# Kernel tuning notes

Hardware: AMD Instinct MI355X
Metric: run time of the kernel (lower is better)

Reference implementation:

```python
import jax, jax.numpy as jnp
import numpy as np

B, S, D, V = 2, 2048, 1024, 32000
EPS_LN = 1e-5
EPS_BN = 1e-5


def setup_inputs() -> dict:
    key = jax.random.key(0)
    ks = jax.random.split(key, 8)
    s = lambda k, shape: jax.random.normal(k, shape, jnp.float32) * 0.02
    return dict(
        X=jax.random.randint(ks[0], (B, S), 0, V, dtype=jnp.int32),
        emb=s(ks[1], (V, D)),
        w_hg=s(ks[2], (D, 2 * D)),            # minGRU to_hidden_and_gate (bias-free)
        conv_w=s(ks[3], (D, D, 3)),           # Conv1d OIW
        conv_b=jnp.zeros((D,), jnp.float32),
        bn_g=jnp.ones((D,), jnp.float32), bn_b=jnp.zeros((D,), jnp.float32),
        ln_g=jnp.ones((D,), jnp.float32), ln_b=jnp.zeros((D,), jnp.float32),
        w1=s(ks[4], (D, 2 * D)), b1=jnp.zeros((2 * D,), jnp.float32),
        w2=s(ks[5], (2 * D, 2 * D)), b2=jnp.zeros((2 * D,), jnp.float32),
        w3=s(ks[6], (2 * D, V)), b3=jnp.zeros((V,), jnp.float32),
    )


def _log_g(x):
    # log of g(x) = where(x>=0, x+0.5, sigmoid(x))
    return jnp.where(x >= 0, jnp.log(jax.nn.relu(x) + 0.5), -jax.nn.softplus(-x))


def _min_gru(x, w_hg):
    # Heinsen log-space associative scan (lucidrains minGRU, expansion=1)
    hg = x @ w_hg                              # [B,S,2D]
    hidden, gate = jnp.split(hg, 2, axis=-1)
    log_coeffs = -jax.nn.softplus(gate)        # log(1 - z)
    log_values = -jax.nn.softplus(-gate) + _log_g(hidden)  # log z + log h~
    a_star = jnp.cumsum(log_coeffs, axis=1)
    log_h = a_star + jax.lax.cumlogsumexp(log_values - a_star, axis=1)
    return jnp.exp(log_h)                      # [B,S,D]


def reference(X, emb, w_hg, conv_w, conv_b, bn_g, bn_b, ln_g, ln_b,
              w1, b1, w2, b2, w3, b3):
    x = emb[X]                                 # [B,S,D]
    shortcut = x
    h = _min_gru(x, w_hg)                      # dropout rate 0 -> identity
    mu = jnp.mean(h, axis=-1, keepdims=True)
    var = jnp.mean((h - mu) ** 2, axis=-1, keepdims=True)
    h = (h - mu) / jnp.sqrt(var + EPS_LN) * ln_g + ln_b
    x = h + shortcut
    xc = jnp.transpose(x, (0, 2, 1))           # [B,D,S]
    xc = jax.lax.conv_general_dilated(
        xc, conv_w, window_strides=(1,), padding=[(1, 1)],
        dimension_numbers=('NCW', 'OIW', 'NCW')) + conv_b[None, :, None]
    m = jnp.mean(xc, axis=(0, 2), keepdims=True)       # BN training-mode stats
    v = jnp.mean((xc - m) ** 2, axis=(0, 2), keepdims=True)
    xc = (xc - m) / jnp.sqrt(v + EPS_BN) * bn_g[None, :, None] + bn_b[None, :, None]
    x = jnp.transpose(xc, (0, 2, 1))           # [B,S,D]
    x = jax.nn.relu(x @ w1 + b1)
    x = jax.nn.relu(x @ w2 + b2)
    return x @ w3 + b3                         # [B,S,V]
```

## Files before the change

### kernel.cpp

```cpp
#include <hip/hip_runtime.h>
#include <hip/hip_bf16.h>

#define B_  2
#define S_  2048
#define D_  1024
#define V_  32000
#define BS_ 4096

typedef __attribute__((ext_vector_type(4))) float f32x4;
typedef __attribute__((ext_vector_type(8))) short short8;
typedef unsigned long long u64;
typedef unsigned short u16;

__device__ __forceinline__ u16 f2bf(float x) {
  unsigned int u = __float_as_uint(x);
  u += 0x7FFFu + ((u >> 16) & 1u);
  return (u16)(u >> 16);
}
__device__ __forceinline__ u64 pack4bf(float a, float b, float c, float d) {
  return (u64)f2bf(a) | ((u64)f2bf(b) << 16) | ((u64)f2bf(c) << 32) | ((u64)f2bf(d) << 48);
}

#define GLOAD_LDS16(g, l) __builtin_amdgcn_global_load_lds( \
    (const __attribute__((address_space(1))) void*)(g),     \
    (__attribute__((address_space(3))) void*)(l), 16, 0, 0)

__device__ __forceinline__ unsigned lds_addr32(const void* p) {
  return (unsigned)(uintptr_t)(const __attribute__((address_space(3))) void*)p;
}
__device__ __forceinline__ short8 ds_read128(unsigned a) {
  short8 r;
  asm volatile("ds_read_b128 %0, %1" : "=&v"(r) : "v"(a));
  return r;
}

template<bool RELU, bool BF16OUT, bool HASBIAS>
__global__ __launch_bounds__(256) void gemm_bt(
    const u16* __restrict__ A, const u16* __restrict__ Bt,
    const float* __restrict__ bias, void* __restrict__ Cout,
    int M, int N, int K)
{
  __shared__ __attribute__((aligned(16))) u16 Alds[128 * 64];
  __shared__ __attribute__((aligned(16))) u16 Blds[128 * 64];
  const int tid = threadIdx.x;
  const int w = tid >> 6, l = tid & 63;
  const int wr = w >> 1, wc = w & 1;
  const int m0 = blockIdx.y * 128, n0 = blockIdx.x * 128;
  const int lr = l >> 3, lc = l & 7;
  const int fr = l & 15, fq = l >> 4;

  const u16* Ag = A + (size_t)(m0 + w * 8 + lr) * K + lc * 8;
  const u16* Bg = Bt + (size_t)(n0 + w * 8 + lr) * K + lc * 8;

  f32x4 acc[4][4];
#pragma unroll
  for (int i = 0; i < 4; ++i)
#pragma unroll
    for (int j = 0; j < 4; ++j) acc[i][j] = {0.f, 0.f, 0.f, 0.f};

  for (int kt = 0; kt < K; kt += 64) {
#pragma unroll
    for (int r = 0; r < 4; ++r) {
      GLOAD_LDS16(Ag + (size_t)(r * 32) * K + kt, &Alds[(r * 32 + w * 8) * 64]);
      GLOAD_LDS16(Bg + (size_t)(r * 32) * K + kt, &Blds[(r * 32 + w * 8) * 64]);
    }
    __syncthreads();
#pragma unroll
    for (int ks = 0; ks < 2; ++ks) {
      short8 af[4], bfv[4];
#pragma unroll
      for (int i = 0; i < 4; ++i)
        af[i] = *reinterpret_cast<const short8*>(
            &Alds[(wr * 64 + i * 16 + fr) * 64 + ks * 32 + fq * 8]);
#pragma unroll
      for (int j = 0; j < 4; ++j)
        bfv[j] = *reinterpret_cast<const short8*>(
            &Blds[(wc * 64 + j * 16 + fr) * 64 + ks * 32 + fq * 8]);
#pragma unroll
      for (int i = 0; i < 4; ++i)
#pragma unroll
        for (int j = 0; j < 4; ++j)
          acc[i][j] = __builtin_amdgcn_mfma_f32_16x16x32_bf16(af[i], bfv[j], acc[i][j], 0, 0, 0);
    }
    __syncthreads();
  }

  const int row0 = m0 + wr * 64 + fq * 4;
  const int col0 = n0 + wc * 64 + fr;
#pragma unroll
  for (int j = 0; j < 4; ++j) {
    const int col = col0 + j * 16;
    const float bv = HASBIAS ? bias[col] : 0.f;
#pragma unroll
    for (int i = 0; i < 4; ++i) {
#pragma unroll
      for (int r = 0; r < 4; ++r) {
        const int row = row0 + i * 16 + r;
        float v = acc[i][j][r] + bv;
        if (RELU) v = fmaxf(v, 0.f);
        if (BF16OUT) ((u16*)Cout)[(size_t)row * N + col] = f2bf(v);
        else         ((float*)Cout)[(size_t)row * N + col] = v;
      }
    }
  }
}

#define AOFF(b, h) (((b) * 4 + (h)) * 8192)
#define BOFF(b, h) (((b) * 4 + 2 + (h)) * 8192)
#define BARRIER() __builtin_amdgcn_s_barrier()
#define WAITL0_PIN() do { asm volatile("s_waitcnt lgkmcnt(0)" ::: "memory"); \
                          __builtin_amdgcn_sched_barrier(0); } while (0)

template<bool RELU, bool BF16OUT, bool HASBIAS>
__global__ __launch_bounds__(512, 2) void gemm256_bt(
    const u16* __restrict__ A, const u16* __restrict__ Bt,
    const float* __restrict__ bias, void* __restrict__ Cout,
    int M, int N, int K, int CW)
{
  __shared__ __attribute__((aligned(16))) u16 LDS[65536];
  const int tid = threadIdx.x;
  const int w = tid >> 6, l = tid & 63;
  const int wr = w >> 2, wc = w & 3;
  const int fr = l & 15, fq = l >> 4;
  const unsigned ldsb = lds_addr32(&LDS[0]);

  const int MTt = M >> 8;
  const int bpc = MTt * CW;
  const int chunk = blockIdx.x / bpc, rem = blockIdx.x % bpc;
  const int m0 = (rem % MTt) << 8;
  const int n0 = ((chunk * CW) + rem / MTt) << 8;

  const int NT = K >> 6;
  const u16* Abase = A + (size_t)m0 * K;
  const u16* Bbase = Bt + (size_t)n0 * K;

  const int rq_[2] = { w * 16 + (l >> 3), w * 16 + 8 + (l >> 3) };
  const int gq_[2] = { (l & 7) ^ (rq_[0] & 7), (l & 7) ^ (rq_[1] & 7) };

#define STAGE_HALF(matbase, h, t, ldsoff) do {                               \
  _Pragma("unroll")                                                          \
  for (int q_ = 0; q_ < 2; ++q_)                                             \
    GLOAD_LDS16((matbase) + ((size_t)((h) * 128 + rq_[q_])) * K +            \
                    (size_t)(t) * 64 + gq_[q_] * 8,                          \
                &LDS[(ldsoff) + (w * 128 + q_ * 64) * 8]);                   \
} while (0)

#define READ_A(arr, bufb, q_) do {                                           \
  _Pragma("unroll")                                                          \
  for (int i_ = 0; i_ < 4; ++i_) {                                           \
    const int r_ = (q_) * 64 + i_ * 16 + fr;                                 \
    _Pragma("unroll")                                                        \
    for (int ks_ = 0; ks_ < 2; ++ks_)                                        \
      arr[i_][ks_] = ds_read128(ldsb + 2u * (unsigned)(AOFF(bufb, wr) +      \
          r_ * 64 + ((ks_ * 4 + fq) ^ (fr & 7)) * 8));                       \
  } } while (0)

#define READ_B(arr, bufb, jq_) do {                                          \
  _Pragma("unroll")                                                          \
  for (int j_ = 0; j_ < 2; ++j_) {                                           \
    const int r_ = (wc & 1) * 64 + (jq_) * 32 + j_ * 16 + fr;                \
    _Pragma("unroll")                                                        \
    for (int ks_ = 0; ks_ < 2; ++ks_)                                        \
      arr[j_][ks_] = ds_read128(ldsb + 2u * (unsigned)(BOFF(bufb, wc >> 1) + \
          r_ * 64 + ((ks_ * 4 + fq) ^ (fr & 7)) * 8));                       \
  } } while (0)

#define MFMA_Q(arrA, arrB, itb, jtb) do {                                    \
  _Pragma("unroll")                                                          \
  for (int i_ = 0; i_ < 4; ++i_)                                             \
    _Pragma("unroll")                                                        \
    for (int j_ = 0; j_ < 2; ++j_)                                           \
      _Pragma("unroll")                                                      \
      for (int ks_ = 0; ks_ < 2; ++ks_)                                      \
        acc[(itb) + i_][(jtb) + j_] = __builtin_amdgcn_mfma_f32_16x16x32_bf16( \
            arrA[i_][ks_], arrB[j_][ks_], acc[(itb) + i_][(jtb) + j_], 0, 0, 0); \
} while (0)

  f32x4 acc[8][4];
#pragma unroll
  for (int i = 0; i < 8; ++i)
#pragma unroll
    for (int j = 0; j < 4; ++j) acc[i][j] = {0.f, 0.f, 0.f, 0.f};

  STAGE_HALF(Abase, 0, 0, AOFF(0, 0));
  STAGE_HALF(Abase, 1, 0, AOFF(0, 1));
  STAGE_HALF(Bbase, 0, 0, BOFF(0, 0));
  STAGE_HALF(Bbase, 1, 0, BOFF(0, 1));
  if (NT > 1) {
    STAGE_HALF(Bbase, 0, 1, BOFF(1, 0));
    STAGE_HALF(Abase, 0, 1, AOFF(1, 0));
    asm volatile("s_waitcnt vmcnt(4)" ::: "memory");
  } else {
    asm volatile("s_waitcnt vmcnt(0)" ::: "memory");
  }
  BARRIER();

  for (int t = 0; t < NT; ++t) {
    const int cb = t & 1, nb = cb ^ 1;
    short8 a0[4][2], a1[4][2], b0[2][2], b1[2][2];

    READ_A(a0, cb, 0);
    READ_B(b0, cb, 0);
    if (t + 1 < NT) STAGE_HALF(Abase, 1, t + 1, AOFF(nb, 1));
    BARRIER(); WAITL0_PIN();
    __builtin_amdgcn_s_setprio(1);
    MFMA_Q(a0, b0, 0, 0);
    __builtin_amdgcn_s_setprio(0);
    BARRIER();

    READ_B(b1, cb, 1);
    if (t + 1 < NT) STAGE_HALF(Bbase, 1, t + 1, BOFF(nb, 1));
    BARRIER(); WAITL0_PIN();
    __builtin_amdgcn_s_setprio(1);
    MFMA_Q(a0, b1, 0, 2);
    __builtin_amdgcn_s_setprio(0);
    BARRIER();

    READ_A(a1, cb, 1);
    if (t + 2 < NT) STAGE_HALF(Bbase, 0, t + 2, BOFF(cb, 0));
    BARRIER(); WAITL0_PIN();
    __builtin_amdgcn_s_setprio(1);
    MFMA_Q(a1, b1, 4, 2);
    __builtin_amdgcn_s_setprio(0);
    BARRIER();

    if (t + 2 < NT) STAGE_HALF(Abase, 0, t + 2, AOFF(cb, 0));
    BARRIER(); WAITL0_PIN();
    __builtin_amdgcn_s_setprio(1);
    MFMA_Q(a1, b0, 4, 0);
    __builtin_amdgcn_s_setprio(0);
    if (t + 2 < NT) { asm volatile("s_waitcnt vmcnt(4)" ::: "memory"); }
    else            { asm volatile("s_waitcnt vmcnt(0)" ::: "memory"); }
    BARRIER();
  }

  float* lf = (float*)(void*)(&LDS[0]) + (size_t)w * 1088;
  const int row_base = m0 + wr * 128;
  const int col_base = n0 + wc * 64;
  float bvv[4];
#pragma unroll
  for (int jt = 0; jt < 4; ++jt)
    bvv[jt] = HASBIAS ? bias[col_base + jt * 16 + fr] : 0.f;
  const int er = l >> 4, ec = (l & 15) * 4;
#pragma unroll
  for (int it = 0; it < 8; ++it) {
#pragma unroll
    for (int jt = 0; jt < 4; ++jt)
#pragma unroll
      for (int rr = 0; rr < 4; ++rr)
        lf[(fq * 4 + rr) * 68 + jt * 16 + fr] = acc[it][jt][rr] + bvv[jt];
#pragma unroll
    for (int ch = 0; ch < 4; ++ch) {
      f32x4 vv = *(const f32x4*)&lf[(ch * 4 + er) * 68 + ec];
      if (RELU) {
        vv[0] = fmaxf(vv[0], 0.f); vv[1] = fmaxf(vv[1], 0.f);
        vv[2] = fmaxf(vv[2], 0.f); vv[3] = fmaxf(vv[3], 0.f);
      }
      const int grow = row_base + it * 16 + ch * 4 + er;
      if (BF16OUT) {
        *(u64*)(&((u16*)Cout)[(size_t)grow * N + col_base + ec]) =
            pack4bf(vv[0], vv[1], vv[2], vv[3]);
      } else {
        *(f32x4*)(&((float*)Cout)[(size_t)grow * N + col_base + ec]) = vv;
      }
    }
    __syncthreads();
  }
#undef STAGE_HALF
#undef READ_A
#undef READ_B
#undef MFMA_Q
}

__global__ __launch_bounds__(256) void transpose_f2b(
    const float* __restrict__ in, u16* __restrict__ out, int K, int N)
{
  __shared__ float t[32][33];
  const int n0 = blockIdx.x * 32, k0 = blockIdx.y * 32;
  const int r = threadIdx.x >> 5, cc = threadIdx.x & 31;
#pragma unroll
  for (int rr = 0; rr < 4; ++rr) {
    const int ki = rr * 8 + r;
    t[ki][cc] = in[(size_t)(k0 + ki) * N + n0 + cc];
  }
  __syncthreads();
#pragma unroll
  for (int rr = 0; rr < 4; ++rr) {
    const int ni = rr * 8 + r;
    out[(size_t)(n0 + ni) * K + k0 + cc] = f2bf(t[cc][ni]);
  }
}

__global__ __launch_bounds__(256) void convw_reorder(
    const float* __restrict__ cw, u16* __restrict__ out)
{
  const int gid = blockIdx.x * 256 + threadIdx.x;
  const int o = gid >> 10, i = gid & 1023;
  const float w0 = cw[(size_t)gid * 3 + 0];
  const float w1 = cw[(size_t)gid * 3 + 1];
  const float w2 = cw[(size_t)gid * 3 + 2];
  out[(size_t)o * 3072 + i]          = f2bf(w0);
  out[(size_t)o * 3072 + 1024 + i]   = f2bf(w1);
  out[(size_t)o * 3072 + 2048 + i]   = f2bf(w2);
}

__global__ __launch_bounds__(256) void gather_emb(
    const int* __restrict__ X, const float* __restrict__ emb, u16* __restrict__ xb)
{
  const int row = blockIdx.x;
  const int tok = X[row];
  const int d4 = threadIdx.x * 4;
  const float4 v = *reinterpret_cast<const float4*>(emb + (size_t)tok * D_ + d4);
  *(u64*)(&xb[(size_t)row * D_ + d4]) = pack4bf(v.x, v.y, v.z, v.w);
}

#define GRU_CP(hid_, gate_, h_, cp_) {                                   \
  const float t_ = __expf(-(gate_));                                     \
  const float z_ = 1.f / (1.f + t_);                                     \
  const float c_ = t_ * z_;                                              \
  const float g_ = ((hid_) >= 0.f) ? ((hid_) + 0.5f)                     \
                                   : (1.f / (1.f + __expf(-(hid_))));    \
  (h_) = c_ * (h_) + z_ * g_; (cp_) *= c_; }

#define GRU_NC(hid_, gate_, h_) {                                        \
  const float t_ = __expf(-(gate_));                                     \
  const float z_ = 1.f / (1.f + t_);                                     \
  const float g_ = ((hid_) >= 0.f) ? ((hid_) + 0.5f)                     \
                                   : (1.f / (1.f + __expf(-(hid_))));    \
  (h_) = (t_ * z_) * (h_) + z_ * g_; }

__global__ __launch_bounds__(256) void scan_partial(
    const float* __restrict__ hg, float* __restrict__ Cb, float* __restrict__ Vb)
{
  const int b = blockIdx.x >> 6, c = blockIdx.x & 63;
  const int d4 = threadIdx.x * 4;
  const float* base = hg + ((size_t)b * S_ + (size_t)c * 32) * (2 * D_);
  float h[4] = {0.f, 0.f, 0.f, 0.f}, cp[4] = {1.f, 1.f, 1.f, 1.f};
  for (int t = 0; t < 32; ++t) {
    const float4 hd = *reinterpret_cast<const float4*>(base + (size_t)t * (2 * D_) + d4);
    const float4 gt = *reinterpret_cast<const float4*>(base + (size_t)t * (2 * D_) + D_ + d4);
    GRU_CP(hd.x, gt.x, h[0], cp[0]); GRU_CP(hd.y, gt.y, h[1], cp[1]);
    GRU_CP(hd.z, gt.z, h[2], cp[2]); GRU_CP(hd.w, gt.w, h[3], cp[3]);
  }
  const size_t o = ((size_t)(b * 64 + c)) * D_ + d4;
  *(float4*)(Cb + o) = make_float4(cp[0], cp[1], cp[2], cp[3]);
  *(float4*)(Vb + o) = make_float4(h[0], h[1], h[2], h[3]);
}

__global__ void scan_carry(const float* __restrict__ Cb, const float* __restrict__ Vb,
                           float* __restrict__ Hs)
{
  const int gid = blockIdx.x * 256 + threadIdx.x;
  const int b = gid >> 10, d = gid & 1023;
  float h = 0.f;
  for (int c = 0; c < 64; ++c) {
    const size_t o = ((size_t)(b * 64 + c)) * D_ + d;
    Hs[o] = h;
    h = Cb[o] * h + Vb[o];
  }
}

__global__ __launch_bounds__(256) void scan_emit(
    const float* __restrict__ hg, const float* __restrict__ Hs,
    const int* __restrict__ X, const float* __restrict__ emb,
    const float* __restrict__ ln_g, const float* __restrict__ ln_b,
    u16* __restrict__ Aconv)
{
  __shared__ float red[4];
  const int b = blockIdx.x >> 6, c = blockIdx.x & 63;
  const int tid = threadIdx.x;
  const int w = tid >> 6, l = tid & 63;
  const int d4 = tid * 4;
  const float* base = hg + ((size_t)b * S_ + (size_t)c * 32) * (2 * D_);
  float h0, h1, h2, h3;
  {
    const float4 hs = *reinterpret_cast<const float4*>(Hs + ((size_t)(b * 64 + c)) * D_ + d4);
    h0 = hs.x; h1 = hs.y; h2 = hs.z; h3 = hs.w;
  }
  const float4 lg = *reinterpret_cast<const float4*>(ln_g + d4);
  const float4 lb = *reinterpret_cast<const float4*>(ln_b + d4);

  for (int t = 0; t < 32; ++t) {
    const int s = c * 32 + t;
    const float4 hd = *reinterpret_cast<const float4*>(base + (size_t)t * (2 * D_) + d4);
    const float4 gt = *reinterpret_cast<const float4*>(base + (size_t)t * (2 * D_) + D_ + d4);
    GRU_NC(hd.x, gt.x, h0); GRU_NC(hd.y, gt.y, h1);
    GRU_NC(hd.z, gt.z, h2); GRU_NC(hd.w, gt.w, h3);

    float sm = h0 + h1 + h2 + h3;
#pragma unroll
    for (int m = 1; m < 64; m <<= 1) sm += __shfl_xor(sm, m);
    __syncthreads();
    if (l == 0) red[w] = sm;
    __syncthreads();
    const float mu = (red[0] + red[1] + red[2] + red[3]) * (1.f / (float)D_);
    float q = (h0 - mu) * (h0 - mu) + (h1 - mu) * (h1 - mu) +
              (h2 - mu) * (h2 - mu) + (h3 - mu) * (h3 - mu);
#pragma unroll
    for (int m = 1; m < 64; m <<= 1) q += __shfl_xor(q, m);
    __syncthreads();
    if (l == 0) red[w] = q;
    __syncthreads();
    const float var = (red[0] + red[1] + red[2] + red[3]) * (1.f / (float)D_);
    const float rstd = rsqrtf(var + 1e-5f);

    const int tok = X[b * S_ + s];
    const float4 e = *reinterpret_cast<const float4*>(emb + (size_t)tok * D_ + d4);
    const float x0 = (h0 - mu) * rstd * lg.x + lb.x + e.x;
    const float x1 = (h1 - mu) * rstd * lg.y + lb.y + e.y;
    const float x2 = (h2 - mu) * rstd * lg.z + lb.z + e.z;
    const float x3 = (h3 - mu) * rstd * lg.w + lb.w + e.w;
    const u64 pk = pack4bf(x0, x1, x2, x3);

    const size_t row = (size_t)b * S_ + s;
    *(u64*)(&Aconv[row * 3072 + D_ + d4]) = pk;
    if (s + 1 < S_) *(u64*)(&Aconv[(row + 1) * 3072 + d4]) = pk;
    if (s > 0)      *(u64*)(&Aconv[(row - 1) * 3072 + 2 * D_ + d4]) = pk;
    if (s == 0)       *(u64*)(&Aconv[row * 3072 + d4]) = 0ull;
    if (s == S_ - 1)  *(u64*)(&Aconv[row * 3072 + 2 * D_ + d4]) = 0ull;
  }
}

__global__ __launch_bounds__(256) void bn_partial(
    const float* __restrict__ cv, float* __restrict__ ps, float* __restrict__ pq)
{
  const int blk = blockIdx.x;
  const int c4 = threadIdx.x * 4;
  float s0 = 0, s1 = 0, s2 = 0, s3 = 0, q0 = 0, q1 = 0, q2 = 0, q3 = 0;
  for (int r = 0; r < 64; ++r) {
    const float4 v = *reinterpret_cast<const float4*>(cv + ((size_t)blk * 64 + r) * D_ + c4);
    s0 += v.x; s1 += v.y; s2 += v.z; s3 += v.w;
    q0 += v.x * v.x; q1 += v.y * v.y; q2 += v.z * v.z; q3 += v.w * v.w;
  }
  *(float4*)(ps + (size_t)blk * D_ + c4) = make_float4(s0, s1, s2, s3);
  *(float4*)(pq + (size_t)blk * D_ + c4) = make_float4(q0, q1, q2, q3);
}

__global__ void bn_finalize(const float* __restrict__ ps, const float* __restrict__ pq,
                            const float* __restrict__ bn_g, const float* __restrict__ bn_b,
                            float* __restrict__ scale, float* __restrict__ shift)
{
  const int c = blockIdx.x * 256 + threadIdx.x;
  float s = 0.f, q = 0.f;
  for (int blk = 0; blk < 64; ++blk) { s += ps[(size_t)blk * D_ + c]; q += pq[(size_t)blk * D_ + c]; }
  const float m = s * (1.f / (float)BS_);
  const float var = q * (1.f / (float)BS_) - m * m;
  const float rs = rsqrtf(var + 1e-5f);
  const float sc = bn_g[c] * rs;
  scale[c] = sc;
  shift[c] = bn_b[c] - m * sc;
}

__global__ __launch_bounds__(256) void bn_apply(
    const float* __restrict__ cv, const float* __restrict__ scale,
    const float* __restrict__ shift, u16* __restrict__ out)
{
  const size_t idx = ((size_t)blockIdx.x * 256 + threadIdx.x) * 4;
  const int c = (int)(idx & 1023);
  const float4 v = *reinterpret_cast<const float4*>(cv + idx);
  const float4 sc = *reinterpret_cast<const float4*>(scale + c);
  const float4 sh = *reinterpret_cast<const float4*>(shift + c);
  *(u64*)(&out[idx]) = pack4bf(v.x * sc.x + sh.x, v.y * sc.y + sh.y,
                               v.z * sc.z + sh.z, v.w * sc.w + sh.w);
}

extern "C" void kernel_launch(void* const* d_in, const int* in_sizes, int n_in,
                              void* d_out, int out_size, void* d_ws, size_t ws_size,
                              hipStream_t stream)
{
  const int*   X      = (const int*)d_in[0];
  const float* emb    = (const float*)d_in[1];
  const float* w_hg   = (const float*)d_in[2];
  const float* conv_w = (const float*)d_in[3];
  const float* bn_g   = (const float*)d_in[5];
  const float* bn_b   = (const float*)d_in[6];
  const float* ln_g   = (const float*)d_in[7];
  const float* ln_b   = (const float*)d_in[8];
  const float* w1     = (const float*)d_in[9];
  const float* b1     = (const float*)d_in[10];
  const float* w2     = (const float*)d_in[11];
  const float* b2     = (const float*)d_in[12];
  const float* w3     = (const float*)d_in[13];
  const float* b3     = (const float*)d_in[14];
  float* out = (float*)d_out;
  char* ws = (char*)d_ws;

  const size_t OFF_A4    = 0;
  const size_t BASE      = 16777216;
  const size_t OFF_W3T   = BASE;
  const size_t OFF_WHGT  = BASE;
  const size_t OFF_W1T   = BASE + 4194304;
  const size_t OFF_W2T   = OFF_W1T + 4194304;
  const size_t OFF_WCVT  = OFF_W2T + 8388608;
  const size_t OFF_XBF   = OFF_WCVT + 6291456;
  const size_t OFF_HG    = OFF_XBF + 8388608;
  const size_t OFF_CB    = OFF_HG + 33554432;
  const size_t OFF_VB    = OFF_CB + 524288;
  const size_t OFF_HS    = OFF_VB + 524288;
  const size_t OFF_ACONV = OFF_HS + 524288;
  const size_t OFF_CVO   = OFF_ACONV + 25165824;
  const size_t OFF_A2    = OFF_CVO + 16777216;
  const size_t OFF_A3    = OFF_A2 + 8388608;
  const size_t OFF_BNS   = OFF_A3 + 16777216;
  const size_t OFF_BNQ   = OFF_BNS + 262144;
  const size_t OFF_SC    = OFF_BNQ + 262144;
  const size_t OFF_SH    = OFF_SC + 4096;
  (void)in_sizes; (void)n_in; (void)out_size; (void)ws_size;

  u16*   WHGT = (u16*)(ws + OFF_WHGT);
  u16*   W1T  = (u16*)(ws + OFF_W1T);
  u16*   W2T  = (u16*)(ws + OFF_W2T);
  u16*   W3T  = (u16*)(ws + OFF_W3T);
  u16*   WCVT = (u16*)(ws + OFF_WCVT);
  u16*   XBF  = (u16*)(ws + OFF_XBF);
  float* HG   = (float*)(ws + OFF_HG);
  float* CB   = (float*)(ws + OFF_CB);
  float* VB   = (float*)(ws + OFF_VB);
  float* HS   = (float*)(ws + OFF_HS);
  u16*   ACONV= (u16*)(ws + OFF_ACONV);
  float* CVO  = (float*)(ws + OFF_CVO);
  u16*   A2   = (u16*)(ws + OFF_A2);
  u16*   A3   = (u16*)(ws + OFF_A3);
  u16*   A4   = (u16*)(ws + OFF_A4);
  float* BNS  = (float*)(ws + OFF_BNS);
  float* BNQ  = (float*)(ws + OFF_BNQ);
  float* SC   = (float*)(ws + OFF_SC);
  float* SH   = (float*)(ws + OFF_SH);

  transpose_f2b<<<dim3(2048 / 32, 1024 / 32), 256, 0, stream>>>(w_hg, WHGT, 1024, 2048);
  transpose_f2b<<<dim3(2048 / 32, 1024 / 32), 256, 0, stream>>>(w1,   W1T,  1024, 2048);
  transpose_f2b<<<dim3(2048 / 32, 2048 / 32), 256, 0, stream>>>(w2,   W2T,  2048, 2048);
  convw_reorder<<<4096, 256, 0, stream>>>(conv_w, WCVT);

  gather_emb<<<BS_, 256, 0, stream>>>(X, emb, XBF);

  gemm_bt<false, false, false><<<dim3(2048 / 128, BS_ / 128), 256, 0, stream>>>(
      XBF, WHGT, nullptr, HG, BS_, 2048, 1024);

  scan_partial<<<B_ * 64, 256, 0, stream>>>(HG, CB, VB);
  scan_carry<<<8, 256, 0, stream>>>(CB, VB, HS);
  scan_emit<<<B_ * 64, 256, 0, stream>>>(HG, HS, X, emb, ln_g, ln_b, ACONV);

  gemm_bt<false, false, false><<<dim3(1024 / 128, BS_ / 128), 256, 0, stream>>>(
      ACONV, WCVT, nullptr, CVO, BS_, 1024, 3072);

  bn_partial<<<64, 256, 0, stream>>>(CVO, BNS, BNQ);
  bn_finalize<<<4, 256, 0, stream>>>(BNS, BNQ, bn_g, bn_b, SC, SH);
  bn_apply<<<4096, 256, 0, stream>>>(CVO, SC, SH, A2);

  gemm_bt<true, true, true><<<dim3(2048 / 128, BS_ / 128), 256, 0, stream>>>(
      A2, W1T, b1, A3, BS_, 2048, 1024);
  gemm_bt<true, true, true><<<dim3(2048 / 128, BS_ / 128), 256, 0, stream>>>(
      A3, W2T, b2, A4, BS_, 2048, 2048);

  transpose_f2b<<<dim3(V_ / 32, 2048 / 32), 256, 0, stream>>>(w3, W3T, 2048, V_);
  gemm256_bt<false, false, true><<<dim3((BS_ / 256) * (V_ / 256)), 512, 0, stream>>>(
      A4, W3T, b3, out, BS_, V_, 2048, 16);
}
```

Baseline: 891.2 us.

## Software-pipeline LDS fragment reads ahead of MFMA phases in 256x256 GEMM

Restructures the main loop of the 256-tile GEMM so each phase issues the LDS reads for the next fragment set before running the current MFMA block. The next tile's first fragments are preloaded at the end of the previous tile, and the loop is unrolled by two with precomputed global and LDS addresses. The epilogue uses a wider padded staging stride, drops the per-row-block __syncthreads, and writes fp32 output with nontemporal stores. The unroll assumes an even K/64 and drops the NT>1 guard, and register pressure rises from the prefetched fragments.

```diff
diff --git a/kernel.cpp b/kernel.cpp
--- a/kernel.cpp
+++ b/kernel.cpp
@@ -30,7 +30,7 @@
 }
 __device__ __forceinline__ short8 ds_read128(unsigned a) {
   short8 r;
-  asm volatile("ds_read_b128 %0, %1" : "=&v"(r) : "v"(a));
+  asm volatile("ds_read_b128 %0, %1" : "=v"(r) : "v"(a));
   return r;
 }
 
@@ -105,11 +105,11 @@
   }
 }
 
-#define AOFF(b, h) (((b) * 4 + (h)) * 8192)
-#define BOFF(b, h) (((b) * 4 + 2 + (h)) * 8192)
 #define BARRIER() __builtin_amdgcn_s_barrier()
 #define WAITL0_PIN() do { asm volatile("s_waitcnt lgkmcnt(0)" ::: "memory"); \
                           __builtin_amdgcn_sched_barrier(0); } while (0)
+#define SCHED_WALL() __builtin_amdgcn_sched_barrier(0)
+#define VMCNTN(n) asm volatile("s_waitcnt vmcnt(" #n ")" ::: "memory")
 
 template<bool RELU, bool BF16OUT, bool HASBIAS>
 __global__ __launch_bounds__(512, 2) void gemm256_bt(
@@ -136,37 +136,48 @@
 
   const int rq_[2] = { w * 16 + (l >> 3), w * 16 + 8 + (l >> 3) };
   const int gq_[2] = { (l & 7) ^ (rq_[0] & 7), (l & 7) ^ (rq_[1] & 7) };
-
-#define STAGE_HALF(matbase, h, t, ldsoff) do {                               \
-  _Pragma("unroll")                                                          \
+  const u16* gA[2][2];
+  const u16* gB[2][2];
+#pragma unroll
+  for (int h = 0; h < 2; ++h)
+#pragma unroll
+    for (int q = 0; q < 2; ++q) {
+      gA[h][q] = Abase + (size_t)(h * 128 + rq_[q]) * K + gq_[q] * 8;
+      gB[h][q] = Bbase + (size_t)(h * 128 + rq_[q]) * K + gq_[q] * 8;
+    }
+
+  const int swz0 = ((0 * 4 + fq) ^ (fr & 7)) * 16;
+  const int swz1 = ((1 * 4 + fq) ^ (fr & 7)) * 16;
+  const unsigned aB = ldsb + 16384u * wr + 128u * fr;
+  const unsigned bB = ldsb + 32768u + 16384u * (wc >> 1) + 128u * ((wc & 1) * 64 + fr);
+  const unsigned bA00 = aB + swz0,           bA01 = aB + swz1;
+  const unsigned bA10 = aB + 65536u + swz0,  bA11 = aB + 65536u + swz1;
+  const unsigned bB00 = bB + swz0,           bB01 = bB + swz1;
+  const unsigned bB10 = bB + 65536u + swz0,  bB11 = bB + 65536u + swz1;
+
+#define STAGE_A(h, t, buf) do { _Pragma("unroll")                            \
   for (int q_ = 0; q_ < 2; ++q_)                                             \
-    GLOAD_LDS16((matbase) + ((size_t)((h) * 128 + rq_[q_])) * K +            \
-                    (size_t)(t) * 64 + gq_[q_] * 8,                          \
-                &LDS[(ldsoff) + (w * 128 + q_ * 64) * 8]);                   \
+    GLOAD_LDS16(gA[h][q_] + (size_t)(t) * 64,                                \
+                &LDS[(((buf) * 4) + (h)) * 8192 + (w * 128 + q_ * 64) * 8]); \
 } while (0)
-
-#define READ_A(arr, bufb, q_) do {                                           \
-  _Pragma("unroll")                                                          \
+#define STAGE_B(h, t, buf) do { _Pragma("unroll")                            \
+  for (int q_ = 0; q_ < 2; ++q_)                                             \
+    GLOAD_LDS16(gB[h][q_] + (size_t)(t) * 64,                                \
+                &LDS[(((buf) * 4) + 2 + (h)) * 8192 + (w * 128 + q_ * 64) * 8]); \
+} while (0)
+
+#define RDA_(arr, k0, k1, Q) do { _Pragma("unroll")                          \
   for (int i_ = 0; i_ < 4; ++i_) {                                           \
-    const int r_ = (q_) * 64 + i_ * 16 + fr;                                 \
-    _Pragma("unroll")                                                        \
-    for (int ks_ = 0; ks_ < 2; ++ks_)                                        \
-      arr[i_][ks_] = ds_read128(ldsb + 2u * (unsigned)(AOFF(bufb, wr) +      \
-          r_ * 64 + ((ks_ * 4 + fq) ^ (fr & 7)) * 8));                       \
+    arr[i_][0] = ds_read128((k0) + (Q) * 8192 + i_ * 2048);                  \
+    arr[i_][1] = ds_read128((k1) + (Q) * 8192 + i_ * 2048);                  \
   } } while (0)
-
-#define READ_B(arr, bufb, jq_) do {                                          \
-  _Pragma("unroll")                                                          \
+#define RDB_(arr, k0, k1, JQ) do { _Pragma("unroll")                         \
   for (int j_ = 0; j_ < 2; ++j_) {                                           \
-    const int r_ = (wc & 1) * 64 + (jq_) * 32 + j_ * 16 + fr;                \
-    _Pragma("unroll")                                                        \
-    for (int ks_ = 0; ks_ < 2; ++ks_)                                        \
-      arr[j_][ks_] = ds_read128(ldsb + 2u * (unsigned)(BOFF(bufb, wc >> 1) + \
-          r_ * 64 + ((ks_ * 4 + fq) ^ (fr & 7)) * 8));                       \
+    arr[j_][0] = ds_read128((k0) + (JQ) * 4096 + j_ * 2048);                 \
+    arr[j_][1] = ds_read128((k1) + (JQ) * 4096 + j_ * 2048);                 \
   } } while (0)
 
-#define MFMA_Q(arrA, arrB, itb, jtb) do {                                    \
-  _Pragma("unroll")                                                          \
+#define MFMA_Q(arrA, arrB, itb, jtb) do { _Pragma("unroll")                  \
   for (int i_ = 0; i_ < 4; ++i_)                                             \
     _Pragma("unroll")                                                        \
     for (int j_ = 0; j_ < 2; ++j_)                                           \
@@ -182,59 +193,57 @@
 #pragma unroll
     for (int j = 0; j < 4; ++j) acc[i][j] = {0.f, 0.f, 0.f, 0.f};
 
-  STAGE_HALF(Abase, 0, 0, AOFF(0, 0));
-  STAGE_HALF(Abase, 1, 0, AOFF(0, 1));
-  STAGE_HALF(Bbase, 0, 0, BOFF(0, 0));
-  STAGE_HALF(Bbase, 1, 0, BOFF(0, 1));
-  if (NT > 1) {
-    STAGE_HALF(Bbase, 0, 1, BOFF(1, 0));
-    STAGE_HALF(Abase, 0, 1, AOFF(1, 0));
-    asm volatile("s_waitcnt vmcnt(4)" ::: "memory");
-  } else {
-    asm volatile("s_waitcnt vmcnt(0)" ::: "memory");
-  }
+  short8 a0[4][2], a1[4][2], b0[2][2], b1[2][2];
+
+  STAGE_A(0, 0, 0); STAGE_A(1, 0, 0); STAGE_B(0, 0, 0); STAGE_B(1, 0, 0);
+  STAGE_B(0, 1, 1); STAGE_A(0, 1, 1);
+  VMCNTN(4);
   BARRIER();
-
-  for (int t = 0; t < NT; ++t) {
-    const int cb = t & 1, nb = cb ^ 1;
-    short8 a0[4][2], a1[4][2], b0[2][2], b1[2][2];
-
-    READ_A(a0, cb, 0);
-    READ_B(b0, cb, 0);
-    if (t + 1 < NT) STAGE_HALF(Abase, 1, t + 1, AOFF(nb, 1));
-    BARRIER(); WAITL0_PIN();
-    __builtin_amdgcn_s_setprio(1);
-    MFMA_Q(a0, b0, 0, 0);
-    __builtin_amdgcn_s_setprio(0);
-    BARRIER();
-
-    READ_B(b1, cb, 1);
-    if (t + 1 < NT) STAGE_HALF(Bbase, 1, t + 1, BOFF(nb, 1));
-    BARRIER(); WAITL0_PIN();
-    __builtin_amdgcn_s_setprio(1);
-    MFMA_Q(a0, b1, 0, 2);
-    __builtin_amdgcn_s_setprio(0);
-    BARRIER();
-
-    READ_A(a1, cb, 1);
-    if (t + 2 < NT) STAGE_HALF(Bbase, 0, t + 2, BOFF(cb, 0));
-    BARRIER(); WAITL0_PIN();
-    __builtin_amdgcn_s_setprio(1);
-    MFMA_Q(a1, b1, 4, 2);
-    __builtin_amdgcn_s_setprio(0);
-    BARRIER();
-
-    if (t + 2 < NT) STAGE_HALF(Abase, 0, t + 2, AOFF(cb, 0));
-    BARRIER(); WAITL0_PIN();
-    __builtin_amdgcn_s_setprio(1);
-    MFMA_Q(a1, b0, 4, 0);
-    __builtin_amdgcn_s_setprio(0);
-    if (t + 2 < NT) { asm volatile("s_waitcnt vmcnt(4)" ::: "memory"); }
-    else            { asm volatile("s_waitcnt vmcnt(0)" ::: "memory"); }
-    BARRIER();
-  }
-
-  float* lf = (float*)(void*)(&LDS[0]) + (size_t)w * 1088;
+  RDA_(a0, bA00, bA01, 0);
+  RDB_(b0, bB00, bB01, 0);
+  BARRIER();
+
+#define TILE(t, cb, nb) do {                                                 \
+                                                                     \
+  WAITL0_PIN();                                                              \
+  RDB_(b1, bB##cb##0, bB##cb##1, 1);                                         \
+  if ((t) + 1 < NT) STAGE_A(1, (t) + 1, nb);                                 \
+  SCHED_WALL();                                                              \
+  __builtin_amdgcn_s_setprio(1); MFMA_Q(a0, b0, 0, 0); __builtin_amdgcn_s_setprio(0); \
+  BARRIER();                                                                 \
+                                                                     \
+  WAITL0_PIN();                                                              \
+  RDA_(a1, bA##cb##0, bA##cb##1, 1);                                         \
+  if ((t) + 1 < NT) STAGE_B(1, (t) + 1, nb);                                 \
+  SCHED_WALL();                                                              \
+  __builtin_amdgcn_s_setprio(1); MFMA_Q(a0, b1, 0, 2); __builtin_amdgcn_s_setprio(0); \
+  BARRIER();                                                                 \
+                                                                     \
+  WAITL0_PIN();                                                              \
+  if ((t) + 2 < NT) STAGE_B(0, (t) + 2, cb);                                 \
+  SCHED_WALL();                                                              \
+  __builtin_amdgcn_s_setprio(1); MFMA_Q(a1, b1, 4, 2); __builtin_amdgcn_s_setprio(0); \
+  BARRIER();                                                                 \
+                                                                     \
+  if ((t) + 2 < NT) STAGE_A(0, (t) + 2, cb);                                 \
+  SCHED_WALL();                                                              \
+  __builtin_amdgcn_s_setprio(1); MFMA_Q(a1, b0, 4, 0); __builtin_amdgcn_s_setprio(0); \
+  if ((t) + 2 < NT) { VMCNTN(4); } else { VMCNTN(0); }                       \
+  BARRIER();                \
+  if ((t) + 1 < NT) {                                                        \
+    RDA_(a0, bA##nb##0, bA##nb##1, 0);                                       \
+    RDB_(b0, bB##nb##0, bB##nb##1, 0);                                       \
+  }                                                                          \
+  BARRIER();                                                                 \
+} while (0)
+
+  for (int t = 0; t < NT; t += 2) {
+    TILE(t, 0, 1);
+    TILE(t + 1, 1, 0);
+  }
+#undef TILE
+
+  float* lf = (float*)(void*)(&LDS[0]) + (size_t)w * 1152;
   const int row_base = m0 + wr * 128;
   const int col_base = n0 + wc * 64;
   float bvv[4];
@@ -248,10 +257,10 @@
     for (int jt = 0; jt < 4; ++jt)
 #pragma unroll
       for (int rr = 0; rr < 4; ++rr)
-        lf[(fq * 4 + rr) * 68 + jt * 16 + fr] = acc[it][jt][rr] + bvv[jt];
+        lf[(fq * 4 + rr) * 72 + jt * 16 + fr] = acc[it][jt][rr] + bvv[jt];
 #pragma unroll
     for (int ch = 0; ch < 4; ++ch) {
-      f32x4 vv = *(const f32x4*)&lf[(ch * 4 + er) * 68 + ec];
+      f32x4 vv = *(const f32x4*)&lf[(ch * 4 + er) * 72 + ec];
       if (RELU) {
         vv[0] = fmaxf(vv[0], 0.f); vv[1] = fmaxf(vv[1], 0.f);
         vv[2] = fmaxf(vv[2], 0.f); vv[3] = fmaxf(vv[3], 0.f);
@@ -261,14 +270,15 @@
         *(u64*)(&((u16*)Cout)[(size_t)grow * N + col_base + ec]) =
             pack4bf(vv[0], vv[1], vv[2], vv[3]);
       } else {
-        *(f32x4*)(&((float*)Cout)[(size_t)grow * N + col_base + ec]) = vv;
+        __builtin_nontemporal_store(vv,
+            (f32x4*)(&((float*)Cout)[(size_t)grow * N + col_base + ec]));
       }
     }
-    __syncthreads();
-  }
-#undef STAGE_HALF
-#undef READ_A
-#undef READ_B
+  }
+#undef STAGE_A
+#undef STAGE_B
+#undef RDA_
+#undef RDB_
 #undef MFMA_Q
 }
 
```

New measurement: 1.015 ms. +13.9%, slower.
